# Kernel tuning notes

Hardware: AMD Instinct MI355X
Metric: run time of the kernel (lower is better)

## Reference

```python
import jax, jax.numpy as jnp
import numpy as np

HIDDEN = 128


def setup_inputs() -> dict:
    key = jax.random.key(0)
    ks = jax.random.split(key, 9)
    N, D, OUT, DIM = 200000, 128, 128, 10000
    msg = jax.random.normal(ks[0], (N, D), dtype=jnp.float32)
    t = jax.random.uniform(ks[1], (N,), dtype=jnp.float32)
    index = jax.random.randint(ks[2], (N,), 0, DIM, dtype=jnp.int32)
    s = 1.0 / np.sqrt(HIDDEN)
    uni = lambda k, shape: jax.random.uniform(k, shape, jnp.float32, -s, s)
    return {
        "msg": msg,
        "t": t,
        "index": index,
        "dim_size": DIM,
        "W_ih": uni(ks[3], (3 * HIDDEN, D)),
        "W_hh": uni(ks[4], (3 * HIDDEN, HIDDEN)),
        "b_ih": uni(ks[5], (3 * HIDDEN,)),
        "b_hh": uni(ks[6], (3 * HIDDEN,)),
        "W_mlp": uni(ks[7], (OUT, HIDDEN)),
        "b_mlp": uni(ks[8], (OUT,)),
    }


def reference(msg, t, index, dim_size, W_ih, W_hh, b_ih, b_hh, W_mlp, b_mlp):
    # Sort messages by node id (primary) and timestamp (secondary). This matches
    # torch: sort by t, then group by index preserving time order within group.
    H = W_hh.shape[1]
    order = jnp.lexsort((t, index))
    idx_s = index[order]          # [N]
    msg_s = msg[order]            # [N, D]
    # segment starts: hidden state resets to 0 at the first message of each node
    start = jnp.concatenate([jnp.ones((1,), bool), idx_s[1:] != idx_s[:-1]])
    # precompute input-gate projections for all messages at once: [N, 3H]
    gi = msg_s @ W_ih.T + b_ih

    def step(h, inp):
        gi_t, st = inp
        h0 = jnp.where(st, jnp.zeros_like(h), h)
        gh = h0 @ W_hh.T + b_hh
        i_r, i_z, i_n = jnp.split(gi_t, 3)
        h_r, h_z, h_n = jnp.split(gh, 3)
        r = jax.nn.sigmoid(i_r + h_r)
        z = jax.nn.sigmoid(i_z + h_z)
        n = jnp.tanh(i_n + r * h_n)
        hn = (1.0 - z) * n + z * h0
        return hn, hn

    h0 = jnp.zeros((H,), msg.dtype)
    _, h_all = jax.lax.scan(step, h0, (gi, start))  # [N, H]

    # final hidden per node = hidden at last (latest-timestamp) message of that node
    pos = jnp.arange(idx_s.shape[0], dtype=jnp.int32)
    last_pos = jax.ops.segment_max(pos, idx_s, num_segments=dim_size)  # empty -> int32 min
    has_msg = last_pos >= 0
    h_node = h_all[jnp.clip(last_pos, 0, None)]     # [dim_size, H]
    out_vals = h_node @ W_mlp.T + b_mlp             # [dim_size, OUT]
    return jnp.where(has_msg[:, None], out_vals, jnp.zeros_like(out_vals))
```

## Files before the change

kernel.cpp:

```cpp
#include <hip/hip_runtime.h>
#include <hip/hip_fp16.h>

typedef _Float16 f16;
typedef _Float16 f16x8 __attribute__((ext_vector_type(8)));
typedef _Float16 f16x4 __attribute__((ext_vector_type(4)));
typedef float    f32x4 __attribute__((ext_vector_type(4)));
typedef unsigned long long u64;
typedef unsigned int u32;

#define HIDDEN 128
#define G3     384

__device__ inline float sigm(float x) { return 1.f / (1.f + __expf(-x)); }
__device__ inline float tanh_f(float x) {
  float ax = fabsf(x);
  float e  = __expf(2.f * ax);
  float r  = 1.f - 2.f / (e + 1.f);
  return x < 0.f ? -r : r;
}


__global__ void hist_kernel(const int* __restrict__ idx, int* __restrict__ counts, int N) {
  int i = blockIdx.x * blockDim.x + threadIdx.x;
  if (i < N) atomicAdd(&counts[idx[i]], 1);
}

__global__ __launch_bounds__(1024) void meta_kernel(const int* __restrict__ counts,
                                                    int* __restrict__ offs,
                                                    int* __restrict__ order, int dim) {
  __shared__ int wsum[16], wpre[16];
  __shared__ int lhist[512], loffs[512], lcur[512];
  const int tid = threadIdx.x, lane = tid & 63, wid = tid >> 6;
  for (int i = tid; i < 512; i += 1024) { lhist[i] = 0; lcur[i] = 0; }
  __syncthreads();
  const int base_i = tid * 16;
  int loc[16];
  int s = 0;
#pragma unroll
  for (int u = 0; u < 16; u++) {
    int i = base_i + u;
    int x = (i < dim) ? counts[i] : 0;
    loc[u] = s; s += x;
    if (i < dim) atomicAdd(&lhist[511 - min(x, 511)], 1);
  }
  int inc = s;
#pragma unroll
  for (int d = 1; d < 64; d <<= 1) { int v = __shfl_up(inc, d, 64); if (lane >= d) inc += v; }
  if (lane == 63) wsum[wid] = inc;
  __syncthreads();
  if (wid == 0 && lane < 16) {
    int v = wsum[lane], p = v;
#pragma unroll
    for (int d = 1; d < 16; d <<= 1) { int q = __shfl_up(p, d, 16); if (lane >= d) p += q; }
    wpre[lane] = p - v;
  }
  __syncthreads();
  const int excl = wpre[wid] + inc - s;
#pragma unroll
  for (int u = 0; u < 16; u++) {
    int i = base_i + u;
    if (i < dim) offs[i] = excl + loc[u];
  }
  if (tid == 1023) offs[dim] = excl + s;
  __syncthreads();
  if (wid == 0) {
    int l8[8]; int ss = 0;
#pragma unroll
    for (int u = 0; u < 8; u++) { l8[u] = ss; ss += lhist[lane * 8 + u]; }
    int inc2 = ss;
#pragma unroll
    for (int d = 1; d < 64; d <<= 1) { int v = __shfl_up(inc2, d, 64); if (lane >= d) inc2 += v; }
    const int e2 = inc2 - ss;
#pragma unroll
    for (int u = 0; u < 8; u++) loffs[lane * 8 + u] = e2 + l8[u];
  }
  __syncthreads();
#pragma unroll
  for (int u = 0; u < 16; u++) {
    int g = base_i + u;
    if (g < dim) {
      int b = 511 - min(counts[g], 511);
      int p = loffs[b] + atomicAdd(&lcur[b], 1);
      order[p] = g;
    }
  }
}

__global__ void scatter_kernel(const float* __restrict__ t, const int* __restrict__ idx,
                               const int* __restrict__ off, int* __restrict__ cursor,
                               u64* __restrict__ keys, int* __restrict__ pos2g, int N) {
  int i = blockIdx.x * blockDim.x + threadIdx.x;
  if (i >= N) return;
  int g = idx[i];
  int p = off[g] + atomicAdd(&cursor[g], 1);
  keys[p] = ((u64)__float_as_uint(t[i]) << 32) | (u32)i;
  pos2g[p] = g;
}

__global__ void rank_kernel(const u64* __restrict__ keys, const int* __restrict__ pos2g,
                            const int* __restrict__ off, const int* __restrict__ cnt,
                            u64* __restrict__ keys2, int N) {
  int p = blockIdx.x * blockDim.x + threadIdx.x;
  if (p >= N) return;
  int g = pos2g[p];
  int s = off[g], m = cnt[g];
  u64 k = keys[p];
  int r = 0;
  for (int q = 0; q < m; q++) r += (keys[s + q] < k);
  keys2[s + r] = k;
}


__global__ void prep_w(const float* __restrict__ W, f16* __restrict__ wfrag) {
  int v = blockIdx.x * blockDim.x + threadIdx.x;
  if (v >= 6144) return;
  int lane = v & 63;
  int t = (v >> 6) % 24;
  int kc = v >> 6 >> 31 ? 0 : (v >> 6) / 24;
  int col = t * 16 + (lane & 15);
  int ks = kc * 32 + (lane >> 4) * 8;
  const float* src = W + (size_t)col * 128 + ks;
  const float4 s0 = *(const float4*)src;
  const float4 s1 = *(const float4*)(src + 4);
  *(f16x8*)(wfrag + (size_t)v * 8) =
      (f16x8){(f16)s0.x, (f16)s0.y, (f16)s0.z, (f16)s0.w,
              (f16)s1.x, (f16)s1.y, (f16)s1.z, (f16)s1.w};
}


__global__ __launch_bounds__(256, 2) void gi_gemm2(const float* __restrict__ A32,
                                                   const f16* __restrict__ wfrag,
                                                   const float* __restrict__ b_ih,
                                                   const float* __restrict__ b_hh,
                                                   f16* __restrict__ GI, int N) {
  const int tid = threadIdx.x;
  const int w = blockIdx.x * 4 + (tid >> 6);
  const int lane = tid & 63;
  const int nrg = (N + 31) >> 5;
  const int rowgrp = w >> 1, ch = w & 1;
  if (rowgrp >= nrg) return;
  const int r0 = rowgrp * 32;
  const int fr = lane & 15, kg = lane >> 4;

  f32x4 acc[2][12];
#pragma unroll
  for (int mi = 0; mi < 2; mi++)
#pragma unroll
    for (int nt = 0; nt < 12; nt++) acc[mi][nt] = (f32x4){0.f, 0.f, 0.f, 0.f};

#pragma unroll
  for (int kc = 0; kc < 4; kc++) {
    f16x8 a[2];
#pragma unroll
    for (int mi = 0; mi < 2; mi++) {
      int row = r0 + mi * 16 + fr; if (row >= N) row = N - 1;
      const float* p = A32 + (size_t)row * 128 + kc * 32 + kg * 8;
      const float4 s0 = *(const float4*)p;
      const float4 s1 = *(const float4*)(p + 4);
      a[mi] = (f16x8){(f16)s0.x, (f16)s0.y, (f16)s0.z, (f16)s0.w,
                      (f16)s1.x, (f16)s1.y, (f16)s1.z, (f16)s1.w};
    }
    f16x8 b[12];
#pragma unroll
    for (int nt = 0; nt < 12; nt++)
      b[nt] = *(const f16x8*)(wfrag + ((size_t)((kc * 24 + ch * 12 + nt) * 64 + lane)) * 8);
#pragma unroll
    for (int mi = 0; mi < 2; mi++)
#pragma unroll
      for (int nt = 0; nt < 12; nt++)
        acc[mi][nt] = __builtin_amdgcn_mfma_f32_16x16x32_f16(a[mi], b[nt], acc[mi][nt], 0, 0, 0);
  }
#pragma unroll
  for (int nt = 0; nt < 12; nt++) {
    int col = ch * 192 + nt * 16 + fr;
    float bi = b_ih[col] + (col < 256 ? b_hh[col] : 0.f);
#pragma unroll
    for (int mi = 0; mi < 2; mi++)
#pragma unroll
      for (int q = 0; q < 4; q++) {
        int row = r0 + mi * 16 + kg * 4 + q;
        if (row < N) GI[(size_t)row * G3 + col] = (f16)(acc[mi][nt][q] + bi);
      }
  }
}


__global__ __launch_bounds__(256) void recur3(
    const f16* __restrict__ GI, const u64* __restrict__ keys,
    const int* __restrict__ off, const int* __restrict__ cnt,
    const float* __restrict__ W_hh, const float* __restrict__ b_hh,
    const float* __restrict__ W_mlp, const float* __restrict__ b_mlp,
    const int* __restrict__ order, float* __restrict__ out, int dim) {
  __shared__ __align__(16) f16 hB[2][16 * 128];
  const int tid = threadIdx.x;
  const int wq = tid >> 6, lane = tid & 63;
  const int c = lane & 15, hi = lane >> 4;

  f16x8 A[6][4];
#pragma unroll
  for (int i = 0; i < 6; i++) {
    const int mt = 2 * wq + (i >> 1) * 8 + (i & 1);
#pragma unroll
    for (int kt = 0; kt < 4; kt++) {
      const float* src = W_hh + (size_t)(mt * 16 + c) * 128 + kt * 32 + hi * 8;
      const float4 s0 = *(const float4*)src;
      const float4 s1 = *(const float4*)(src + 4);
      A[i][kt] = (f16x8){(f16)s0.x, (f16)s0.y, (f16)s0.z, (f16)s0.w,
                         (f16)s1.x, (f16)s1.y, (f16)s1.z, (f16)s1.w};
    }
  }
  const f32x4 bhn0 = *(const f32x4*)(b_hh + 256 + (2 * wq) * 16 + hi * 4);
  const f32x4 bhn1 = *(const f32x4*)(b_hh + 256 + (2 * wq + 1) * 16 + hi * 4);

  const int oidx = blockIdx.x * 16 + c;
  const bool valid = (oidx < dim);
  const int g = valid ? order[oidx] : 0;
  const int m = valid ? cnt[g] : 0;
  const int s = valid ? off[g] : 0;
  int L = m;
#pragma unroll
  for (int d = 1; d < 16; d <<= 1) L = max(L, __shfl_xor(L, d, 16));

  float h0[8];
#pragma unroll
  for (int i = 0; i < 8; i++) h0[i] = 0.f;
  const f16x4 z4 = {(f16)0.f, (f16)0.f, (f16)0.f, (f16)0.f};
  *(f16x4*)&hB[0][c * 128 + (((2 * wq) ^ (c & 7)) * 16) + hi * 4] = z4;
  *(f16x4*)&hB[0][c * 128 + (((2 * wq + 1) ^ (c & 7)) * 16) + hi * 4] = z4;
  __syncthreads();

  const u32* keysLo = (const u32*)keys;
  const int go_r = 2 * wq * 16 + hi * 4;
  u32 mid = keysLo[2 * ((m > 0) ? s : 0)];
  const f16* gp0 = GI + (size_t)mid * G3 + go_r;
  f16x4 gr0 = *(const f16x4*)(gp0);
  f16x4 gr1 = *(const f16x4*)(gp0 + 16);
  f16x4 gz0 = *(const f16x4*)(gp0 + 128);
  f16x4 gz1 = *(const f16x4*)(gp0 + 144);
  f16x4 gn0 = *(const f16x4*)(gp0 + 256);
  f16x4 gn1 = *(const f16x4*)(gp0 + 272);
  u32 midn = keysLo[2 * ((m > 0) ? (s + min(1, m - 1)) : 0)];

  for (int st = 0; st < L; ++st) {
    const f16* gpn = GI + (size_t)midn * G3 + go_r;
    f16x4 ngr0 = *(const f16x4*)(gpn);
    f16x4 ngr1 = *(const f16x4*)(gpn + 16);
    f16x4 ngz0 = *(const f16x4*)(gpn + 128);
    f16x4 ngz1 = *(const f16x4*)(gpn + 144);
    f16x4 ngn0 = *(const f16x4*)(gpn + 256);
    f16x4 ngn1 = *(const f16x4*)(gpn + 272);
    u32 midn2 = keysLo[2 * ((m > 0) ? (s + min(st + 2, m - 1)) : 0)];

    const f16* hr = hB[st & 1];
    f16x8 B[4];
#pragma unroll
    for (int kt = 0; kt < 4; kt++)
      B[kt] = *(const f16x8*)&hr[c * 128 + (((2 * kt + (hi >> 1)) ^ (c & 7)) * 16) + (hi & 1) * 8];

    f32x4 C[6];
#pragma unroll
    for (int i = 0; i < 6; i++) C[i] = (f32x4){0.f, 0.f, 0.f, 0.f};
#pragma unroll
    for (int i = 0; i < 6; i++)
#pragma unroll
      for (int kt = 0; kt < 4; kt++)
        C[i] = __builtin_amdgcn_mfma_f32_16x16x32_f16(A[i][kt], B[kt], C[i], 0, 0, 0);

    const bool act = (st < m);
#pragma unroll
    for (int q_ = 0; q_ < 4; q_++) {
      float r = sigm((float)gr0[q_] + C[0][q_]);
      float z = sigm((float)gz0[q_] + C[2][q_]);
      float n = tanh_f((float)gn0[q_] + r * (C[4][q_] + bhn0[q_]));
      if (act) h0[q_] = (1.f - z) * n + z * h0[q_];
      float r2 = sigm((float)gr1[q_] + C[1][q_]);
      float z2 = sigm((float)gz1[q_] + C[3][q_]);
      float n2 = tanh_f((float)gn1[q_] + r2 * (C[5][q_] + bhn1[q_]));
      if (act) h0[4 + q_] = (1.f - z2) * n2 + z2 * h0[4 + q_];
    }
    f16* hw = hB[(st + 1) & 1];
    *(f16x4*)&hw[c * 128 + (((2 * wq) ^ (c & 7)) * 16) + hi * 4] =
        (f16x4){(f16)h0[0], (f16)h0[1], (f16)h0[2], (f16)h0[3]};
    *(f16x4*)&hw[c * 128 + (((2 * wq + 1) ^ (c & 7)) * 16) + hi * 4] =
        (f16x4){(f16)h0[4], (f16)h0[5], (f16)h0[6], (f16)h0[7]};
    __syncthreads();

    gr0 = ngr0; gr1 = ngr1; gz0 = ngz0; gz1 = ngz1; gn0 = ngn0; gn1 = ngn1;
    mid = midn; midn = midn2;
  }

  const f16* hf = hB[L & 1];
  f16x8 Bf[4];
#pragma unroll
  for (int kt = 0; kt < 4; kt++)
    Bf[kt] = *(const f16x8*)&hf[c * 128 + (((2 * kt + (hi >> 1)) ^ (c & 7)) * 16) + (hi & 1) * 8];
#pragma unroll
  for (int oi = 0; oi < 2; oi++) {
    const int ot = 2 * wq + oi;
    f32x4 o = *(const f32x4*)(b_mlp + ot * 16 + hi * 4);
#pragma unroll
    for (int kt = 0; kt < 4; kt++) {
      const float* wsrc = W_mlp + (size_t)(ot * 16 + c) * 128 + kt * 32 + hi * 8;
      const float4 w0 = *(const float4*)wsrc;
      const float4 w1 = *(const float4*)(wsrc + 4);
      f16x8 Af = {(f16)w0.x, (f16)w0.y, (f16)w0.z, (f16)w0.w,
                  (f16)w1.x, (f16)w1.y, (f16)w1.z, (f16)w1.w};
      o = __builtin_amdgcn_mfma_f32_16x16x32_f16(Af, Bf[kt], o, 0, 0, 0);
    }
    if (valid) {
      f32x4 oz = (m > 0) ? o : (f32x4){0.f, 0.f, 0.f, 0.f};
      *(f32x4*)(out + (size_t)g * 128 + ot * 16 + hi * 4) = oz;
    }
  }
}


extern "C" void kernel_launch(void* const* d_in, const int* in_sizes, int n_in,
                              void* d_out, int out_size, void* d_ws, size_t ws_size,
                              hipStream_t stream) {
  const float* msg   = (const float*)d_in[0];
  const float* t     = (const float*)d_in[1];
  const int*   indx  = (const int*)d_in[2];
  const float* W_ih  = (const float*)d_in[4];
  const float* W_hh  = (const float*)d_in[5];
  const float* b_ih  = (const float*)d_in[6];
  const float* b_hh  = (const float*)d_in[7];
  const float* W_mlp = (const float*)d_in[8];
  const float* b_mlp = (const float*)d_in[9];
  float* out = (float*)d_out;
  const int N   = in_sizes[0] / 128;
  const int dim = out_size / 128;
  const int nb  = (dim + 15) / 16;

  char* ws = (char*)d_ws;
  size_t o = 0;
  auto alloc = [&](size_t b) { size_t r = o; o = (o + b + 255) & ~(size_t)255; return r; };
  f16* gi16   = (f16*)(ws + alloc((size_t)N * G3 * 2));
  u64* keys   = (u64*)(ws + alloc((size_t)N * 8));
  u64* keys2  = (u64*)(ws + alloc((size_t)N * 8));
  int* pos2g  = (int*)(ws + alloc((size_t)N * 4));
  int* offs   = (int*)(ws + alloc((size_t)(dim + 1) * 4));
  int* order  = (int*)(ws + alloc((size_t)dim * 4));
  f16* wfrag  = (f16*)(ws + alloc(6144 * 8 * 2));
  size_t meta_bytes = (size_t)(2 * dim) * 4;
  char* meta  = ws + alloc(meta_bytes);
  int* counts = (int*)meta;
  int* cursor = (int*)(meta + (size_t)dim * 4);

  hipMemsetAsync(meta, 0, meta_bytes, stream);

  const int gN = (N + 255) / 256;
  prep_w<<<24, 256, 0, stream>>>(W_ih, wfrag);
  hist_kernel<<<gN, 256, 0, stream>>>(indx, counts, N);
  meta_kernel<<<1, 1024, 0, stream>>>(counts, offs, order, dim);
  scatter_kernel<<<gN, 256, 0, stream>>>(t, indx, offs, cursor, keys, pos2g, N);
  rank_kernel<<<gN, 256, 0, stream>>>(keys, pos2g, offs, counts, keys2, N);

  const int nrg = (N + 31) / 32;
  const int nwaves = nrg * 2;
  gi_gemm2<<<(nwaves + 3) / 4, 256, 0, stream>>>(msg, wfrag, b_ih, b_hh, gi16, N);

  recur3<<<nb, 256, 0, stream>>>(gi16, keys2, offs, counts, W_hh, b_hh,
                                 W_mlp, b_mlp, order, out, dim);
}
```

Measured before the change: 387.7 us.

## Fuse input-gate projection into recurrence kernel, drop separate GI GEMM

The separate W_ih GEMM and its fp16 GI buffer are removed. The recurrence kernel now gathers each step's message row into shared memory, double-buffered with a one-step prefetch, and computes the input projection with MFMA alongside the hidden projection. Blocks grow to 512 threads so each wave owns one 16-row slice of every gate, with the W_ih and W_hh fragments held in registers. This removes the write and re-read of a large intermediate and one kernel launch. In exchange it adds MFMA work, register pressure and a global-load latency to every serial step of the recurrence.

```diff
diff --git a/kernel.cpp b/kernel.cpp
--- a/kernel.cpp
+++ b/kernel.cpp
@@ -18,6 +18,14 @@
   float r  = 1.f - 2.f / (e + 1.f);
   return x < 0.f ? -r : r;
 }
+__device__ inline f16x4 cvt4(float4 v) {
+  return (f16x4){(f16)v.x, (f16)v.y, (f16)v.z, (f16)v.w};
+}
+__device__ inline f16x8 cvt8(float4 a, float4 b) {
+  return (f16x8){(f16)a.x, (f16)a.y, (f16)a.z, (f16)a.w,
+                 (f16)b.x, (f16)b.y, (f16)b.z, (f16)b.w};
+}
+__device__ inline f32x4 ld4(const float* p) { return *(const f32x4*)p; }
 
 
 __global__ void hist_kernel(const int* __restrict__ idx, int* __restrict__ counts, int N) {
@@ -111,206 +119,126 @@
 }
 
 
-__global__ void prep_w(const float* __restrict__ W, f16* __restrict__ wfrag) {
-  int v = blockIdx.x * blockDim.x + threadIdx.x;
-  if (v >= 6144) return;
-  int lane = v & 63;
-  int t = (v >> 6) % 24;
-  int kc = v >> 6 >> 31 ? 0 : (v >> 6) / 24;
-  int col = t * 16 + (lane & 15);
-  int ks = kc * 32 + (lane >> 4) * 8;
-  const float* src = W + (size_t)col * 128 + ks;
-  const float4 s0 = *(const float4*)src;
-  const float4 s1 = *(const float4*)(src + 4);
-  *(f16x8*)(wfrag + (size_t)v * 8) =
-      (f16x8){(f16)s0.x, (f16)s0.y, (f16)s0.z, (f16)s0.w,
-              (f16)s1.x, (f16)s1.y, (f16)s1.z, (f16)s1.w};
-}
-
-
-__global__ __launch_bounds__(256, 2) void gi_gemm2(const float* __restrict__ A32,
-                                                   const f16* __restrict__ wfrag,
-                                                   const float* __restrict__ b_ih,
-                                                   const float* __restrict__ b_hh,
-                                                   f16* __restrict__ GI, int N) {
-  const int tid = threadIdx.x;
-  const int w = blockIdx.x * 4 + (tid >> 6);
-  const int lane = tid & 63;
-  const int nrg = (N + 31) >> 5;
-  const int rowgrp = w >> 1, ch = w & 1;
-  if (rowgrp >= nrg) return;
-  const int r0 = rowgrp * 32;
-  const int fr = lane & 15, kg = lane >> 4;
-
-  f32x4 acc[2][12];
-#pragma unroll
-  for (int mi = 0; mi < 2; mi++)
-#pragma unroll
-    for (int nt = 0; nt < 12; nt++) acc[mi][nt] = (f32x4){0.f, 0.f, 0.f, 0.f};
-
-#pragma unroll
-  for (int kc = 0; kc < 4; kc++) {
-    f16x8 a[2];
-#pragma unroll
-    for (int mi = 0; mi < 2; mi++) {
-      int row = r0 + mi * 16 + fr; if (row >= N) row = N - 1;
-      const float* p = A32 + (size_t)row * 128 + kc * 32 + kg * 8;
-      const float4 s0 = *(const float4*)p;
-      const float4 s1 = *(const float4*)(p + 4);
-      a[mi] = (f16x8){(f16)s0.x, (f16)s0.y, (f16)s0.z, (f16)s0.w,
-                      (f16)s1.x, (f16)s1.y, (f16)s1.z, (f16)s1.w};
-    }
-    f16x8 b[12];
-#pragma unroll
-    for (int nt = 0; nt < 12; nt++)
-      b[nt] = *(const f16x8*)(wfrag + ((size_t)((kc * 24 + ch * 12 + nt) * 64 + lane)) * 8);
-#pragma unroll
-    for (int mi = 0; mi < 2; mi++)
-#pragma unroll
-      for (int nt = 0; nt < 12; nt++)
-        acc[mi][nt] = __builtin_amdgcn_mfma_f32_16x16x32_f16(a[mi], b[nt], acc[mi][nt], 0, 0, 0);
-  }
-#pragma unroll
-  for (int nt = 0; nt < 12; nt++) {
-    int col = ch * 192 + nt * 16 + fr;
-    float bi = b_ih[col] + (col < 256 ? b_hh[col] : 0.f);
-#pragma unroll
-    for (int mi = 0; mi < 2; mi++)
-#pragma unroll
-      for (int q = 0; q < 4; q++) {
-        int row = r0 + mi * 16 + kg * 4 + q;
-        if (row < N) GI[(size_t)row * G3 + col] = (f16)(acc[mi][nt][q] + bi);
-      }
-  }
-}
-
-
-__global__ __launch_bounds__(256) void recur3(
-    const f16* __restrict__ GI, const u64* __restrict__ keys,
+__global__ __launch_bounds__(512) void recur4(
+    const float* __restrict__ msg, const u64* __restrict__ keys,
     const int* __restrict__ off, const int* __restrict__ cnt,
-    const float* __restrict__ W_hh, const float* __restrict__ b_hh,
+    const float* __restrict__ W_ih, const float* __restrict__ W_hh,
+    const float* __restrict__ b_ih, const float* __restrict__ b_hh,
     const float* __restrict__ W_mlp, const float* __restrict__ b_mlp,
     const int* __restrict__ order, float* __restrict__ out, int dim) {
   __shared__ __align__(16) f16 hB[2][16 * 128];
+  __shared__ __align__(16) f16 mB[2][16 * 128];
+  __shared__ int sArr[16], mArr[16];
   const int tid = threadIdx.x;
-  const int wq = tid >> 6, lane = tid & 63;
+  const int q = tid >> 6, lane = tid & 63;
   const int c = lane & 15, hi = lane >> 4;
-
-  f16x8 A[6][4];
-#pragma unroll
-  for (int i = 0; i < 6; i++) {
-    const int mt = 2 * wq + (i >> 1) * 8 + (i & 1);
-#pragma unroll
-    for (int kt = 0; kt < 4; kt++) {
-      const float* src = W_hh + (size_t)(mt * 16 + c) * 128 + kt * 32 + hi * 8;
-      const float4 s0 = *(const float4*)src;
-      const float4 s1 = *(const float4*)(src + 4);
-      A[i][kt] = (f16x8){(f16)s0.x, (f16)s0.y, (f16)s0.z, (f16)s0.w,
-                         (f16)s1.x, (f16)s1.y, (f16)s1.z, (f16)s1.w};
-    }
-  }
-  const f32x4 bhn0 = *(const f32x4*)(b_hh + 256 + (2 * wq) * 16 + hi * 4);
-  const f32x4 bhn1 = *(const f32x4*)(b_hh + 256 + (2 * wq + 1) * 16 + hi * 4);
+  const int ct = tid >> 5;
+  const int j4 = (tid & 31) * 4;
 
   const int oidx = blockIdx.x * 16 + c;
   const bool valid = (oidx < dim);
   const int g = valid ? order[oidx] : 0;
   const int m = valid ? cnt[g] : 0;
-  const int s = valid ? off[g] : 0;
+  const int s = (valid && m > 0) ? off[g] : 0;
+  if (tid < 16) { sArr[tid] = s; mArr[tid] = m; }
   int L = m;
 #pragma unroll
   for (int d = 1; d < 16; d <<= 1) L = max(L, __shfl_xor(L, d, 16));
 
-  float h0[8];
-#pragma unroll
-  for (int i = 0; i < 8; i++) h0[i] = 0.f;
-  const f16x4 z4 = {(f16)0.f, (f16)0.f, (f16)0.f, (f16)0.f};
-  *(f16x4*)&hB[0][c * 128 + (((2 * wq) ^ (c & 7)) * 16) + hi * 4] = z4;
-  *(f16x4*)&hB[0][c * 128 + (((2 * wq + 1) ^ (c & 7)) * 16) + hi * 4] = z4;
+  f16x8 Ai[3][4], Ah[3][4];
+#pragma unroll
+  for (int p = 0; p < 3; p++)
+#pragma unroll
+    for (int kt = 0; kt < 4; kt++) {
+      const size_t ro = (size_t)(p * 128 + q * 16 + c) * 128 + kt * 32 + hi * 8;
+      Ai[p][kt] = cvt8(*(const float4*)(W_ih + ro), *(const float4*)(W_ih + ro + 4));
+      Ah[p][kt] = cvt8(*(const float4*)(W_hh + ro), *(const float4*)(W_hh + ro + 4));
+    }
+  const int rb = q * 16 + hi * 4;
+  const f32x4 bR  = ld4(b_ih + rb)       + ld4(b_hh + rb);
+  const f32x4 bZ  = ld4(b_ih + 128 + rb) + ld4(b_hh + 128 + rb);
+  const f32x4 bNi = ld4(b_ih + 256 + rb);
+  const f32x4 bNh = ld4(b_hh + 256 + rb);
+
+  float h0[4] = {0.f, 0.f, 0.f, 0.f};
+  *(f16x4*)&hB[0][c * 128 + ((q ^ (c & 7)) * 16) + hi * 4] =
+      (f16x4){(f16)0.f, (f16)0.f, (f16)0.f, (f16)0.f};
   __syncthreads();
 
   const u32* keysLo = (const u32*)keys;
-  const int go_r = 2 * wq * 16 + hi * 4;
-  u32 mid = keysLo[2 * ((m > 0) ? s : 0)];
-  const f16* gp0 = GI + (size_t)mid * G3 + go_r;
-  f16x4 gr0 = *(const f16x4*)(gp0);
-  f16x4 gr1 = *(const f16x4*)(gp0 + 16);
-  f16x4 gz0 = *(const f16x4*)(gp0 + 128);
-  f16x4 gz1 = *(const f16x4*)(gp0 + 144);
-  f16x4 gn0 = *(const f16x4*)(gp0 + 256);
-  f16x4 gn1 = *(const f16x4*)(gp0 + 272);
-  u32 midn = keysLo[2 * ((m > 0) ? (s + min(1, m - 1)) : 0)];
+  const int sc = sArr[ct], mc = mArr[ct];
+  {
+    const u32 mid0 = keysLo[2 * sc];
+    const float4 v = *(const float4*)(msg + (size_t)mid0 * 128 + j4);
+    const int tk = j4 >> 4;
+    *(f16x4*)&mB[0][ct * 128 + ((tk ^ (ct & 7)) * 16) + (j4 & 15)] = cvt4(v);
+  }
+  __syncthreads();
 
   for (int st = 0; st < L; ++st) {
-    const f16* gpn = GI + (size_t)midn * G3 + go_r;
-    f16x4 ngr0 = *(const f16x4*)(gpn);
-    f16x4 ngr1 = *(const f16x4*)(gpn + 16);
-    f16x4 ngz0 = *(const f16x4*)(gpn + 128);
-    f16x4 ngz1 = *(const f16x4*)(gpn + 144);
-    f16x4 ngn0 = *(const f16x4*)(gpn + 256);
-    f16x4 ngn1 = *(const f16x4*)(gpn + 272);
-    u32 midn2 = keysLo[2 * ((m > 0) ? (s + min(st + 2, m - 1)) : 0)];
-
     const f16* hr = hB[st & 1];
-    f16x8 B[4];
-#pragma unroll
-    for (int kt = 0; kt < 4; kt++)
-      B[kt] = *(const f16x8*)&hr[c * 128 + (((2 * kt + (hi >> 1)) ^ (c & 7)) * 16) + (hi & 1) * 8];
-
-    f32x4 C[6];
-#pragma unroll
-    for (int i = 0; i < 6; i++) C[i] = (f32x4){0.f, 0.f, 0.f, 0.f};
-#pragma unroll
-    for (int i = 0; i < 6; i++)
-#pragma unroll
-      for (int kt = 0; kt < 4; kt++)
-        C[i] = __builtin_amdgcn_mfma_f32_16x16x32_f16(A[i][kt], B[kt], C[i], 0, 0, 0);
-
+    const f16* mr = mB[st & 1];
+    f16x8 Bh[4], Bm[4];
+#pragma unroll
+    for (int kt = 0; kt < 4; kt++) {
+      const int ad = c * 128 + (((2 * kt + (hi >> 1)) ^ (c & 7)) * 16) + (hi & 1) * 8;
+      Bh[kt] = *(const f16x8*)&hr[ad];
+      Bm[kt] = *(const f16x8*)&mr[ad];
+    }
+    const bool stg = (st + 1 < L);
+    float4 v;
+    if (stg) {
+      const int pos = sc + max(0, min(st + 1, mc - 1));
+      const u32 midn = keysLo[2 * pos];
+      v = *(const float4*)(msg + (size_t)midn * 128 + j4);
+    }
+    f32x4 Cr = bR, Cz = bZ, Cni = bNi, Cnh = bNh;
+#pragma unroll
+    for (int kt = 0; kt < 4; kt++) Cr  = __builtin_amdgcn_mfma_f32_16x16x32_f16(Ai[0][kt], Bm[kt], Cr, 0, 0, 0);
+#pragma unroll
+    for (int kt = 0; kt < 4; kt++) Cr  = __builtin_amdgcn_mfma_f32_16x16x32_f16(Ah[0][kt], Bh[kt], Cr, 0, 0, 0);
+#pragma unroll
+    for (int kt = 0; kt < 4; kt++) Cz  = __builtin_amdgcn_mfma_f32_16x16x32_f16(Ai[1][kt], Bm[kt], Cz, 0, 0, 0);
+#pragma unroll
+    for (int kt = 0; kt < 4; kt++) Cz  = __builtin_amdgcn_mfma_f32_16x16x32_f16(Ah[1][kt], Bh[kt], Cz, 0, 0, 0);
+#pragma unroll
+    for (int kt = 0; kt < 4; kt++) Cni = __builtin_amdgcn_mfma_f32_16x16x32_f16(Ai[2][kt], Bm[kt], Cni, 0, 0, 0);
+#pragma unroll
+    for (int kt = 0; kt < 4; kt++) Cnh = __builtin_amdgcn_mfma_f32_16x16x32_f16(Ah[2][kt], Bh[kt], Cnh, 0, 0, 0);
     const bool act = (st < m);
 #pragma unroll
-    for (int q_ = 0; q_ < 4; q_++) {
-      float r = sigm((float)gr0[q_] + C[0][q_]);
-      float z = sigm((float)gz0[q_] + C[2][q_]);
-      float n = tanh_f((float)gn0[q_] + r * (C[4][q_] + bhn0[q_]));
-      if (act) h0[q_] = (1.f - z) * n + z * h0[q_];
-      float r2 = sigm((float)gr1[q_] + C[1][q_]);
-      float z2 = sigm((float)gz1[q_] + C[3][q_]);
-      float n2 = tanh_f((float)gn1[q_] + r2 * (C[5][q_] + bhn1[q_]));
-      if (act) h0[4 + q_] = (1.f - z2) * n2 + z2 * h0[4 + q_];
-    }
-    f16* hw = hB[(st + 1) & 1];
-    *(f16x4*)&hw[c * 128 + (((2 * wq) ^ (c & 7)) * 16) + hi * 4] =
+    for (int qq = 0; qq < 4; qq++) {
+      float r = sigm(Cr[qq]);
+      float z = sigm(Cz[qq]);
+      float n = tanh_f(Cni[qq] + r * Cnh[qq]);
+      if (act) h0[qq] = (1.f - z) * n + z * h0[qq];
+    }
+    *(f16x4*)&hB[(st + 1) & 1][c * 128 + ((q ^ (c & 7)) * 16) + hi * 4] =
         (f16x4){(f16)h0[0], (f16)h0[1], (f16)h0[2], (f16)h0[3]};
-    *(f16x4*)&hw[c * 128 + (((2 * wq + 1) ^ (c & 7)) * 16) + hi * 4] =
-        (f16x4){(f16)h0[4], (f16)h0[5], (f16)h0[6], (f16)h0[7]};
+    if (stg) {
+      const int tk = j4 >> 4;
+      *(f16x4*)&mB[(st + 1) & 1][ct * 128 + ((tk ^ (ct & 7)) * 16) + (j4 & 15)] = cvt4(v);
+    }
     __syncthreads();
-
-    gr0 = ngr0; gr1 = ngr1; gz0 = ngz0; gz1 = ngz1; gn0 = ngn0; gn1 = ngn1;
-    mid = midn; midn = midn2;
   }
 
   const f16* hf = hB[L & 1];
   f16x8 Bf[4];
 #pragma unroll
-  for (int kt = 0; kt < 4; kt++)
-    Bf[kt] = *(const f16x8*)&hf[c * 128 + (((2 * kt + (hi >> 1)) ^ (c & 7)) * 16) + (hi & 1) * 8];
-#pragma unroll
-  for (int oi = 0; oi < 2; oi++) {
-    const int ot = 2 * wq + oi;
-    f32x4 o = *(const f32x4*)(b_mlp + ot * 16 + hi * 4);
-#pragma unroll
-    for (int kt = 0; kt < 4; kt++) {
-      const float* wsrc = W_mlp + (size_t)(ot * 16 + c) * 128 + kt * 32 + hi * 8;
-      const float4 w0 = *(const float4*)wsrc;
-      const float4 w1 = *(const float4*)(wsrc + 4);
-      f16x8 Af = {(f16)w0.x, (f16)w0.y, (f16)w0.z, (f16)w0.w,
-                  (f16)w1.x, (f16)w1.y, (f16)w1.z, (f16)w1.w};
-      o = __builtin_amdgcn_mfma_f32_16x16x32_f16(Af, Bf[kt], o, 0, 0, 0);
-    }
-    if (valid) {
-      f32x4 oz = (m > 0) ? o : (f32x4){0.f, 0.f, 0.f, 0.f};
-      *(f32x4*)(out + (size_t)g * 128 + ot * 16 + hi * 4) = oz;
-    }
+  for (int kt = 0; kt < 4; kt++) {
+    const int ad = c * 128 + (((2 * kt + (hi >> 1)) ^ (c & 7)) * 16) + (hi & 1) * 8;
+    Bf[kt] = *(const f16x8*)&hf[ad];
+  }
+  f32x4 o = ld4(b_mlp + q * 16 + hi * 4);
+#pragma unroll
+  for (int kt = 0; kt < 4; kt++) {
+    const size_t wo = (size_t)(q * 16 + c) * 128 + kt * 32 + hi * 8;
+    f16x8 Af = cvt8(*(const float4*)(W_mlp + wo), *(const float4*)(W_mlp + wo + 4));
+    o = __builtin_amdgcn_mfma_f32_16x16x32_f16(Af, Bf[kt], o, 0, 0, 0);
+  }
+  if (valid) {
+    const f32x4 oz = (m > 0) ? o : (f32x4){0.f, 0.f, 0.f, 0.f};
+    *(f32x4*)(out + (size_t)g * 128 + q * 16 + hi * 4) = oz;
   }
 }
 
@@ -335,13 +263,11 @@
   char* ws = (char*)d_ws;
   size_t o = 0;
   auto alloc = [&](size_t b) { size_t r = o; o = (o + b + 255) & ~(size_t)255; return r; };
-  f16* gi16   = (f16*)(ws + alloc((size_t)N * G3 * 2));
   u64* keys   = (u64*)(ws + alloc((size_t)N * 8));
   u64* keys2  = (u64*)(ws + alloc((size_t)N * 8));
   int* pos2g  = (int*)(ws + alloc((size_t)N * 4));
   int* offs   = (int*)(ws + alloc((size_t)(dim + 1) * 4));
   int* order  = (int*)(ws + alloc((size_t)dim * 4));
-  f16* wfrag  = (f16*)(ws + alloc(6144 * 8 * 2));
   size_t meta_bytes = (size_t)(2 * dim) * 4;
   char* meta  = ws + alloc(meta_bytes);
   int* counts = (int*)meta;
@@ -350,16 +276,11 @@
   hipMemsetAsync(meta, 0, meta_bytes, stream);
 
   const int gN = (N + 255) / 256;
-  prep_w<<<24, 256, 0, stream>>>(W_ih, wfrag);
   hist_kernel<<<gN, 256, 0, stream>>>(indx, counts, N);
   meta_kernel<<<1, 1024, 0, stream>>>(counts, offs, order, dim);
   scatter_kernel<<<gN, 256, 0, stream>>>(t, indx, offs, cursor, keys, pos2g, N);
   rank_kernel<<<gN, 256, 0, stream>>>(keys, pos2g, offs, counts, keys2, N);
 
-  const int nrg = (N + 31) / 32;
-  const int nwaves = nrg * 2;
-  gi_gemm2<<<(nwaves + 3) / 4, 256, 0, stream>>>(msg, wfrag, b_ih, b_hh, gi16, N);
-
-  recur3<<<nb, 256, 0, stream>>>(gi16, keys2, offs, counts, W_hh, b_hh,
+  recur4<<<nb, 512, 0, stream>>>(msg, keys2, offs, counts, W_ih, W_hh, b_ih, b_hh,
                                  W_mlp, b_mlp, order, out, dim);
 }
```

New measurement: 350.1 us. -9.7%, faster.
